# Kernel tuning notes

Measured on AMD Instinct MI355X. Metric: run time of the kernel, lower is better.

Reference implementation:

```python
import jax, jax.numpy as jnp
import numpy as np

# --- static mask-construction config (mirrors FlexAttnFunc.init_mask args) ---
B = 1
L_F, L_H, L_W = 8, 20, 36      # latent_shape[2:]
A_F, A_H, A_W = 8, 1, 1        # action_shape[2:]
PATCH = (1, 2, 2)
CHUNK = 1
PAD = 176
WINDOW = 6
DIM, HEADS, DHEAD = 1536, 12, 128
EPS = 1e-5


def _make_ids():
    lf, lh, lw = L_F // PATCH[0], L_H // PATCH[1], L_W // PATCH[2]
    lat_seq = np.repeat(np.arange(B), lf * lh * lw)
    act_seq = np.repeat(np.arange(B), A_F * A_H * A_W)
    seq = np.concatenate([lat_seq, lat_seq, act_seq, act_seq])
    lat_fr = np.broadcast_to(np.arange(L_F)[None, :, None, None], (B, L_F, lh, lw)).reshape(-1)
    act_fr = np.broadcast_to(np.arange(A_F)[None, :, None, None], (B, A_F, A_H, A_W)).reshape(-1)
    fr = np.concatenate([lat_fr // CHUNK * 2] * 2 + [act_fr // CHUNK * 2 + 1] * 2)
    nz = np.concatenate([np.zeros_like(lat_fr), np.ones_like(lat_fr),
                         np.zeros_like(act_fr), np.ones_like(act_fr)])
    pad = np.full(PAD, -1, dtype=np.int64)
    return (np.concatenate([seq, pad]).astype(np.int32),
            np.concatenate([fr, pad]).astype(np.int32),
            np.concatenate([nz, pad]).astype(np.int32))


def setup_inputs() -> dict:
    key = jax.random.key(0)
    ks = jax.random.split(key, 8)
    seq, fr, nz = _make_ids()
    S = seq.shape[0]  # 3072
    sd = 0.02
    return {
        'x': jax.random.normal(ks[0], (1, S, DIM), jnp.float32),
        'Wq': jax.random.normal(ks[1], (DIM, DIM), jnp.float32) * sd,
        'bq': jnp.zeros((DIM,), jnp.float32),
        'Wk': jax.random.normal(ks[2], (DIM, DIM), jnp.float32) * sd,
        'bk': jnp.zeros((DIM,), jnp.float32),
        'Wv': jax.random.normal(ks[3], (DIM, DIM), jnp.float32) * sd,
        'bv': jnp.zeros((DIM,), jnp.float32),
        'gq': 1.0 + jax.random.normal(ks[4], (DIM,), jnp.float32) * sd,
        'gk': 1.0 + jax.random.normal(ks[5], (DIM,), jnp.float32) * sd,
        'Wo': jax.random.normal(ks[6], (DIM, DIM), jnp.float32) * sd,
        'bo': jnp.zeros((DIM,), jnp.float32),
        'seq_ids': jnp.asarray(seq),
        'frame_ids': jnp.asarray(fr),
        'noise_ids': jnp.asarray(nz),
        'window_size': WINDOW,
    }


def _rms(u, g):
    # torch.nn.RMSNorm over last dim (size heads*dim_head), elementwise affine
    return u * jax.lax.rsqrt(jnp.mean(u * u, axis=-1, keepdims=True) + EPS) * g


def _mask(seq_ids, frame_ids, noise_ids, window_size):
    sq, sk = seq_ids[:, None], seq_ids[None, :]
    fq, fk = frame_ids[:, None], frame_ids[None, :]
    nq, nk = noise_ids[:, None], noise_ids[None, :]
    seq_ok = (sq == sk) & (sq >= 0) & (sk >= 0)
    c2c = (nq == 1) & (nk == 1) & (fk <= fq)      # clean->clean, block causal incl self
    n2c = (nq == 0) & (nk == 1) & (fk < fq)       # noise->clean, causal excl self
    n2n = (nq == 0) & (nk == 0) & (fk == fq)      # noise->noise, same frame only
    win = jnp.abs(fq - fk) <= window_size
    return (c2c | n2c | n2n) & seq_ok & win


def reference(x, Wq, bq, Wk, bk, Wv, bv, gq, gk, Wo, bo,
              seq_ids, frame_ids, noise_ids, window_size):
    S = x.shape[1]
    q = _rms(x @ Wq + bq, gq)[0].reshape(S, HEADS, DHEAD)
    k = _rms(x @ Wk + bk, gk)[0].reshape(S, HEADS, DHEAD)
    v = (x @ Wv + bv)[0].reshape(S, HEADS, DHEAD)
    mask = _mask(seq_ids, frame_ids, noise_ids, window_size)  # [S,S] bool
    scores = jnp.einsum('qhd,khd->hqk', q, k) * (DHEAD ** -0.5)
    scores = jnp.where(mask[None], scores, jnp.float32(-1e9))
    attn = jax.nn.softmax(scores, axis=-1)
    o = jnp.einsum('hqk,khd->qhd', attn, v)
    # zero out padded (fully-masked) query rows
    o = o * (seq_ids >= 0).astype(o.dtype)[:, None, None]
    y = o.reshape(1, S, HEADS * DHEAD) @ Wo + bo
    return y
```

## Files before the change

kernel.cpp:

```cpp
#include <hip/hip_runtime.h>
#include <hip/hip_bf16.h>
#include <stdint.h>

typedef __bf16 bf16x8 __attribute__((ext_vector_type(8)));
typedef float f32x4 __attribute__((ext_vector_type(4)));

__device__ __forceinline__ unsigned short f2bf(float f) {
  union { float f; unsigned int u; } v; v.f = f;
  unsigned int u = v.u;
  unsigned int r = (u + 0x7fffu + ((u >> 16) & 1u)) >> 16;
  return (unsigned short)r;
}
__device__ __forceinline__ float bf2f(unsigned short s) {
  union { unsigned int u; float f; } v; v.u = ((unsigned int)s) << 16; return v.f;
}

__global__ __launch_bounds__(256) void setup(
    const float* __restrict__ x,
    const float* __restrict__ Wq, const float* __restrict__ Wk,
    const float* __restrict__ Wv, const float* __restrict__ Wo,
    const int* __restrict__ seq, const int* __restrict__ fr,
    const int* __restrict__ nz, const int* __restrict__ wsz,
    unsigned short* __restrict__ x_bf, unsigned short* __restrict__ wt,
    unsigned long long* __restrict__ tbm, unsigned char* __restrict__ mb,
    float* __restrict__ ssq, int* __restrict__ sched, int S) {
  __shared__ __align__(16) unsigned char smu[16384];
  int b = blockIdx.x, tid = threadIdx.x;
  if (b == 0) {
    int* ks_ = (int*)smu;
    unsigned int* tm_ = (unsigned int*)(smu + 12288);
    int* cnt_s = (int*)(smu + 13312);
    int W = wsz[0];
    for (int i = tid; i < S; i += 256) {
      int sq = seq[i];
      ks_[i] = (sq < 0) ? 0 : ((1 << 9) | ((nz[i] & 1) << 8) | (fr[i] & 15) | (sq << 10));
    }
    for (int i = tid; i < 6144; i += 256) ssq[i] = 0.f;
    __syncthreads();
    for (int t = tid; t < S / 32; t += 256) {
      unsigned int m = 0;
      for (int j = 0; j < 32; j++) {
        int a = ks_[t * 32 + j];
        if (a & (1 << 9)) m |= (a & (1 << 8)) ? (1u << (16 + (a & 15))) : (1u << (a & 15));
      }
      tm_[t] = m;
    }
    __syncthreads();
    for (int qg = tid; qg < S / 16; qg += 256) {
      unsigned int allowed = 0;
      for (int j = 0; j < 16; j++) {
        int a = ks_[qg * 16 + j];
        if (!(a & (1 << 9))) continue;
        int fq = a & 15, nq = (a >> 8) & 1;
        int lo = fq - W; if (lo < 0) lo = 0;
        unsigned int lom = ~((1u << lo) - 1);
        if (nq) allowed |= (((1u << (fq + 1)) - 1) & lom) << 16;
        else    allowed |= ((((1u << fq) - 1) & lom) << 16) | (1u << fq);
      }
      unsigned long long b0 = 0, b1 = 0;
      for (int t = 0; t < 96; t++)
        if (tm_[t] & allowed) { if (t < 64) b0 |= 1ull << t; else b1 |= 1ull << (t - 64); }
      tbm[qg * 2] = b0; tbm[qg * 2 + 1] = b1;
    }
    __syncthreads();
    if (tid < 48) {
      unsigned long long u0 = tbm[(tid * 4) * 2]     | tbm[(tid * 4 + 1) * 2] |
                              tbm[(tid * 4 + 2) * 2] | tbm[(tid * 4 + 3) * 2];
      unsigned long long u1 = tbm[(tid * 4) * 2 + 1]     | tbm[(tid * 4 + 1) * 2 + 1] |
                              tbm[(tid * 4 + 2) * 2 + 1] | tbm[(tid * 4 + 3) * 2 + 1];
      cnt_s[tid] = __popcll(u0) + __popcll(u1);
    }
    __syncthreads();
    if (tid < 48) {
      int c = cnt_s[tid], rank = 0;
      for (int j = 0; j < 48; j++) {
        int cj = cnt_s[j];
        if (cj > c || (cj == c && j < tid)) rank++;
      }
      sched[rank] = tid;
    }
  } else if (b < 193) {
    int qg = b - 1;
    int* ks_ = (int*)smu;
    int W = wsz[0];
    for (int i = tid; i < S; i += 256) {
      int sq = seq[i];
      ks_[i] = (sq < 0) ? 0 : ((1 << 9) | ((nz[i] & 1) << 8) | (fr[i] & 15) | (sq << 10));
    }
    __syncthreads();
    int wave = tid >> 6, lane = tid & 63, quad = lane >> 4, l16 = lane & 15;
    int aq[4];
    for (int r = 0; r < 4; r++) aq[r] = ks_[qg * 16 + quad * 4 + r];
    for (int t = wave; t < 96; t += 4) {
      int ak[2] = { ks_[t * 32 + l16], ks_[t * 32 + 16 + l16] };
      unsigned int byte = 0;
      for (int nt = 0; nt < 2; nt++) {
        int a = ak[nt];
        int kfr = a & 15, knz = (a >> 8) & 1, kvb = (a >> 9) & 1, ksq = a >> 10;
        for (int r = 0; r < 4; r++) {
          int bq_ = aq[r];
          int qfr = bq_ & 15, qnz = (bq_ >> 8) & 1, qvb = (bq_ >> 9) & 1, qsq = bq_ >> 10;
          bool ok  = qvb && kvb && (qsq == ksq);
          bool c2c = qnz && knz && (kfr <= qfr);
          bool n2c = !qnz && knz && (kfr < qfr);
          bool n2n = !qnz && !knz && (kfr == qfr);
          int df = qfr - kfr; df = df < 0 ? -df : df;
          if ((c2c || n2c || n2n) && ok && (df <= W)) byte |= 1u << (nt * 4 + r);
        }
      }
      mb[((size_t)qg * 96 + t) * 64 + lane] = (unsigned char)byte;
    }
  } else if (b < 1345) {
    int base = (b - 193) * 1024 + tid;
    for (int j = 0; j < 4; j++) {
      int i = base + j * 256;
      float4 v = ((const float4*)x)[i];
      ushort4 o;
      o.x = f2bf(v.x); o.y = f2bf(v.y); o.z = f2bf(v.z); o.w = f2bf(v.w);
      ((ushort4*)x_bf)[i] = o;
    }
  } else {
    int id = b - 1345;
    int z = id / 576, rem = id % 576;
    int kx = rem % 24, ny = rem / 24;
    const float* W = z == 0 ? Wq : (z == 1 ? Wk : (z == 2 ? Wv : Wo));
    unsigned short (*t)[65] = (unsigned short(*)[65])smu;
    int k0 = kx * 64, n0 = ny * 64;
    const int N = 1536, K = 1536;
    for (int i = 0; i < 4; i++) {
      int e = tid + i * 256;
      int r = e >> 4, c4 = (e & 15) * 4;
      float4 v = *(const float4*)&W[(size_t)(k0 + r) * N + n0 + c4];
      t[c4 + 0][r] = f2bf(v.x);
      t[c4 + 1][r] = f2bf(v.y);
      t[c4 + 2][r] = f2bf(v.z);
      t[c4 + 3][r] = f2bf(v.w);
    }
    __syncthreads();
    for (int i = 0; i < 4; i++) {
      int e = tid + i * 256;
      int c = e >> 4, r4 = (e & 15) * 4;
      ushort4 o;
      o.x = t[c][r4 + 0];
      o.y = t[c][r4 + 1];
      o.z = t[c][r4 + 2];
      o.w = t[c][r4 + 3];
      *(ushort4*)&wt[(size_t)(z * 1536 + n0 + c) * K + k0 + r4] = o;
    }
  }
}

__global__ __launch_bounds__(512) void gemm_qkv(
    const unsigned short* __restrict__ A, const unsigned short* __restrict__ Bt,
    const float* __restrict__ bq, const float* __restrict__ bk, const float* __restrict__ bv,
    const float* __restrict__ gq, const float* __restrict__ gk,
    unsigned short* __restrict__ qt, unsigned short* __restrict__ ktb,
    unsigned short* __restrict__ vtb, float* __restrict__ ssq, int S) {
  __shared__ __align__(16) unsigned short smem[65536];
  int tid = threadIdx.x, wid = tid >> 6, lane = tid & 63;
  int quad = lane >> 4, l16 = lane & 15;
  int m0 = blockIdx.x * 256, n0 = blockIdx.y * 256;
  int wm = (wid >> 2) * 128;
  int wn = (wid & 3) * 64;
  int lr = lane >> 3;
  int lsw = ((lane & 7) ^ lr) * 8;
  int sx = l16 & 7;

  f32x4 acc[8][4] = {};

#define STAGEQ(t_, q_) do { \
    if ((t_) < 24) { \
      int b_ = (t_) & 1; \
      int k0_ = (t_) * 64; \
      unsigned short* ldsb = ((q_) < 2) ? (smem + b_ * 16384) : (smem + 32768 + b_ * 16384); \
      const unsigned short* gsrc = ((q_) < 2) ? A : Bt; \
      int rbase = ((q_) < 2) ? m0 : n0; \
      int lo8_ = ((q_) & 1) * 8; \
      for (int c_ = 0; c_ < 2; c_++) { \
        int chunk = lo8_ + c_ * 16 + wid; \
        const unsigned short* src = gsrc + (size_t)(rbase + chunk * 8 + lr) * 1536 + k0_ + lsw; \
        __builtin_amdgcn_global_load_lds( \
            (const __attribute__((address_space(1))) unsigned int*)src, \
            (__attribute__((address_space(3))) unsigned int*)(ldsb + chunk * 512 + lane * 8), 16, 0, 0); \
      } \
    } } while (0)

  STAGEQ(0, 0); STAGEQ(0, 1); STAGEQ(0, 2); STAGEQ(0, 3);
  STAGEQ(1, 0);
  asm volatile("s_waitcnt vmcnt(2)" ::: "memory");
  __builtin_amdgcn_s_barrier();
  __builtin_amdgcn_sched_barrier(0);

#define PHASE(p) do { \
    constexpr int q_ = (p) & 3; \
    constexpr int tb_ = (p) >> 2; \
    constexpr int k8_ = (q_ >> 1) * 4; \
    constexpr int mi0_ = (q_ & 1) * 4; \
    unsigned short* Ab = smem + tb_ * 16384; \
    unsigned short* Bb = smem + 32768 + tb_ * 16384; \
    int so_ = ((k8_ + quad) ^ sx) << 3; \
    if constexpr ((q_ & 1) == 0) { \
      for (int nj = 0; nj < 4; nj++) \
        bfr[nj] = *(const bf16x8*)&Bb[(wn + nj * 16 + l16) * 64 + so_]; \
    } \
    bf16x8 af[4]; \
    for (int ii = 0; ii < 4; ii++) \
      af[ii] = *(const bf16x8*)&Ab[(wm + (mi0_ + ii) * 16 + l16) * 64 + so_]; \
    STAGEQ(2 * i + kStT[p], kStQ[p]); \
    __builtin_amdgcn_sched_barrier(0); \
    __builtin_amdgcn_s_barrier(); \
    asm volatile("s_waitcnt lgkmcnt(0)" ::: "memory"); \
    __builtin_amdgcn_sched_barrier(0); \
    __builtin_amdgcn_s_setprio(1); \
    for (int ii = 0; ii < 4; ii++) \
      for (int nj = 0; nj < 4; nj++) \
        acc[mi0_ + ii][nj] = __builtin_amdgcn_mfma_f32_16x16x32_bf16(af[ii], bfr[nj], acc[mi0_ + ii][nj], 0, 0, 0); \
    __builtin_amdgcn_s_setprio(0); \
    if constexpr (q_ == 3) { asm volatile("s_waitcnt vmcnt(2)" ::: "memory"); } \
    __builtin_amdgcn_s_barrier(); \
    __builtin_amdgcn_sched_barrier(0); \
  } while (0)

  constexpr int kStT[8] = {1, 1, 1, 2, 2, 2, 2, 3};
  constexpr int kStQ[8] = {1, 2, 3, 0, 1, 2, 3, 0};

  for (int i = 0; i < 12; i++) {
    bf16x8 bfr[4];
    PHASE(0); PHASE(1); PHASE(2); PHASE(3);
    PHASE(4); PHASE(5); PHASE(6); PHASE(7);
  }
#undef PHASE
#undef STAGEQ

  int region = (n0 >= 3072) ? 2 : (n0 >= 1536 ? 1 : 0);
  int cbase = n0 - region * 1536;
  int hh0 = cbase >> 7;
  unsigned short* Cs = smem;
  if (region < 2) {
    const float* bias = region == 0 ? bq : bk;
    float* ssqp = ssq + region * 3072;
    float ss[8][4] = {};
    for (int nj = 0; nj < 4; nj++) {
      int col = wn + nj * 16 + l16;
      float b = bias[cbase + col];
      float G = (region == 1) ? gq[cbase + col] * gk[cbase + col] : 1.0f;
      for (int mi = 0; mi < 8; mi++)
        for (int r = 0; r < 4; r++) {
          float v = acc[mi][nj][r] + b;
          ss[mi][r] += v * v;
          Cs[(wm + mi * 16 + quad * 4 + r) * 256 + col] = f2bf(v * G);
        }
    }
    for (int mi = 0; mi < 8; mi++)
      for (int r = 0; r < 4; r++) {
        float v = ss[mi][r];
        for (int o = 1; o < 16; o <<= 1) v += __shfl_xor(v, o);
        if (l16 == 0)
          atomicAdd(&ssqp[m0 + wm + mi * 16 + quad * 4 + r], v);
      }
    __syncthreads();
    unsigned short* outb = (region == 0 ? qt : ktb);
    for (int p = 0; p < 16; p++) {
      int o = p * 4096 + tid * 8;
      int row = o >> 8, col = o & 255;
      size_t dst = (size_t)(hh0 + (col >> 7)) * 393216 + (size_t)(m0 + row) * 128 + (col & 127);
      *(uint4*)&outb[dst] = *(const uint4*)&Cs[o];
    }
  } else {
    for (int nj = 0; nj < 4; nj++) {
      int col = wn + nj * 16 + l16;
      float b = bv[cbase + col];
      int c8 = l16 * 8;
      for (int mi = 0; mi < 8; mi++)
        for (int r = 0; r < 4; r++) {
          int sp = wm + mi * 16 + quad * 4 + r;
          Cs[col * 256 + (sp ^ c8)] = f2bf(acc[mi][nj][r] + b);
        }
    }
    __syncthreads();
    for (int hh = 0; hh < 2; hh++) {
      unsigned short* outp = vtb + ((size_t)(hh0 + hh) * 96 + (m0 >> 5)) * 4096;
      for (int p = 0; p < 8; p++) {
        int o = p * 4096 + tid * 8;
        int tile = o >> 12, rem = o & 4095;
        int dd = rem >> 5, s31 = rem & 31;
        int laddr = (hh * 128 + dd) * 256 + ((tile * 32 + s31) ^ ((dd & 15) * 8));
        *(uint4*)&outp[o] = *(const uint4*)&Cs[laddr];
      }
    }
  }
}

__global__ __launch_bounds__(256) void gemm_wo(
    const unsigned short* __restrict__ op0b, const unsigned short* __restrict__ op1b,
    const float* __restrict__ lp, const int* __restrict__ seq,
    const unsigned short* __restrict__ Bt,
    const float* __restrict__ bias, float* __restrict__ C, int M, int N, int K) {
  __shared__ __align__(16) unsigned short smem[16384];
  unsigned short* As = smem;
  unsigned short* Bs = smem + 8192;
  int tid = threadIdx.x, wave = tid >> 6, lane = tid & 63;
  int quad = lane >> 4, l16 = lane & 15;
  int m0 = blockIdx.x * 128, n0 = blockIdx.y * 128;
  int wm = (wave & 1) * 64, wn = (wave >> 1) * 64;
  int lr = lane >> 3;
  int lc = ((lane & 7) ^ lr) * 8;
  int sx = l16 & 7;
  f32x4 acc[4][4] = {};
  for (int k0 = 0; k0 < K; k0 += 64) {
    for (int c = 0; c < 4; c++) {
      int chunk = wave * 4 + c;
      int row = chunk * 8 + lr;
      int q = m0 + row;
      int col = k0 + lc;
      int h = col >> 7, dd = col & 127;
      ushort4 a0 = *(const ushort4*)&op0b[((size_t)h * 3072 + q) * 128 + dd];
      ushort4 a1 = *(const ushort4*)&op1b[((size_t)h * 3072 + q) * 128 + dd];
      float l0 = lp[h * 3072 + q], l1 = lp[(12 + h) * 3072 + q];
      float tot = l0 + l1;
      float ok = (seq[q] >= 0 && tot > 0.f) ? 1.0f / tot : 0.0f;
      float w0 = l0 * ok, w1 = l1 * ok;
      ushort4 o;
      o.x = f2bf(bf2f(a0.x) * w0 + bf2f(a1.x) * w1);
      o.y = f2bf(bf2f(a0.y) * w0 + bf2f(a1.y) * w1);
      o.z = f2bf(bf2f(a0.z) * w0 + bf2f(a1.z) * w1);
      o.w = f2bf(bf2f(a0.w) * w0 + bf2f(a1.w) * w1);
      ushort4 a0b = *(const ushort4*)&op0b[((size_t)h * 3072 + q) * 128 + dd + 4];
      ushort4 a1b = *(const ushort4*)&op1b[((size_t)h * 3072 + q) * 128 + dd + 4];
      ushort4 o2;
      o2.x = f2bf(bf2f(a0b.x) * w0 + bf2f(a1b.x) * w1);
      o2.y = f2bf(bf2f(a0b.y) * w0 + bf2f(a1b.y) * w1);
      o2.z = f2bf(bf2f(a0b.z) * w0 + bf2f(a1b.z) * w1);
      o2.w = f2bf(bf2f(a0b.w) * w0 + bf2f(a1b.w) * w1);
      *(ushort4*)&As[chunk * 512 + lane * 8] = o;
      *(ushort4*)&As[chunk * 512 + lane * 8 + 4] = o2;
    }
    for (int c = 0; c < 4; c++) {
      int chunk = wave * 4 + c;
      int row = chunk * 8 + lr;
      const unsigned short* gb = &Bt[(size_t)(n0 + row) * K + k0 + lc];
      __builtin_amdgcn_global_load_lds(
          (const __attribute__((address_space(1))) unsigned int*)gb,
          (__attribute__((address_space(3))) unsigned int*)(Bs + chunk * 512), 16, 0, 0);
    }
    __syncthreads();
    for (int kk = 0; kk < 64; kk += 32) {
      int k8 = kk >> 3;
      int sw = ((k8 + quad) ^ sx) << 3;
      bf16x8 af[4], bfr[4];
      for (int i = 0; i < 4; i++)
        af[i] = *(const bf16x8*)&As[(wm + i * 16 + l16) * 64 + sw];
      for (int j = 0; j < 4; j++)
        bfr[j] = *(const bf16x8*)&Bs[(wn + j * 16 + l16) * 64 + sw];
      for (int i = 0; i < 4; i++)
        for (int j = 0; j < 4; j++)
          acc[i][j] = __builtin_amdgcn_mfma_f32_16x16x32_bf16(af[i], bfr[j], acc[i][j], 0, 0, 0);
    }
    __syncthreads();
  }
  for (int j = 0; j < 4; j++) {
    int col = n0 + wn + j * 16 + l16;
    float b = bias[col];
    for (int i = 0; i < 4; i++)
      for (int r = 0; r < 4; r++)
        C[(size_t)(m0 + wm + i * 16 + quad * 4 + r) * N + col] = acc[i][j][r] + b;
  }
}

__global__ __launch_bounds__(256) void attn(
    const unsigned short* __restrict__ qt,
    const unsigned short* __restrict__ kt,
    const unsigned short* __restrict__ vt,
    const unsigned char* __restrict__ mb,
    const unsigned long long* __restrict__ tbm,
    const float* __restrict__ ssq,
    const int* __restrict__ sched,
    unsigned short* __restrict__ op0b, unsigned short* __restrict__ op1b,
    float* __restrict__ lp, int S) {
  const int h = blockIdx.x;
  const int qb64 = sched[blockIdx.y];
  const int split = blockIdx.z;
  int tid = threadIdx.x, wave = tid >> 6, lane = tid & 63;
  int quad = lane >> 4, l16 = lane & 15;
  const float scale = 0.088388347648318447f;

  __shared__ __align__(16) unsigned short KsF[3 * 4096];
  __shared__ __align__(16) unsigned short VsF[3 * 4096];
  __shared__ __align__(16) unsigned short pshare[4][16][40];

  int qg = qb64 * 4 + wave;
  unsigned long long bm0 = tbm[(qb64 * 4) * 2]     | tbm[(qb64 * 4 + 1) * 2] |
                           tbm[(qb64 * 4 + 2) * 2] | tbm[(qb64 * 4 + 3) * 2];
  unsigned long long bm1 = tbm[(qb64 * 4) * 2 + 1]     | tbm[(qb64 * 4 + 1) * 2 + 1] |
                           tbm[(qb64 * 4 + 2) * 2 + 1] | tbm[(qb64 * 4 + 3) * 2 + 1];
  unsigned long long wb0 = tbm[qg * 2], wb1 = tbm[qg * 2 + 1];

  const unsigned short* kth = kt + (size_t)h * 96 * 4096;
  const unsigned short* vth = vt + (size_t)h * 96 * 4096;
  const unsigned char* mbq = mb + (size_t)qg * 96 * 64;

  bf16x8 qf[4];
  {
    const unsigned short* qp = qt + ((size_t)(h * 192 + qg) * 16 + l16) * 128 + quad * 8;
    for (int ks = 0; ks < 4; ks++) qf[ks] = *(const bf16x8*)&qp[ks * 32];
  }
  float qs[4];
  for (int r = 0; r < 4; r++) {
    int row = qb64 * 64 + wave * 16 + quad * 4 + r;
    qs[r] = rsqrtf(ssq[row] * (1.0f / 1536.0f) + 1e-5f) * scale;
  }
  const float* ssk = ssq + 3072;

  f32x4 oacc[8] = {};
  f32x4 lacc = {};
  const __bf16 onebf = (__bf16)1.0f;
  const bf16x8 ones = {onebf, onebf, onebf, onebf, onebf, onebf, onebf, onebf};

#define POP(dst) do { \
    if (bm0) { dst = __builtin_ctzll(bm0); bm0 &= bm0 - 1; } \
    else if (bm1) { dst = 64 + __builtin_ctzll(bm1); bm1 &= bm1 - 1; } \
    else dst = -1; } while (0)

#define STAGE(t_, b_) do { \
    for (int j = 0; j < 2; j++) { \
      int slot = j * 256 + tid; \
      int key = slot >> 4, cc = slot & 15; \
      const unsigned short* src = kth + (size_t)(t_) * 4096 + key * 128 + (cc ^ (key & 15)) * 8; \
      __builtin_amdgcn_global_load_lds( \
          (const __attribute__((address_space(1))) unsigned int*)src, \
          (__attribute__((address_space(3))) unsigned int*)(&KsF[(b_) * 4096] + j * 2048 + wave * 512), \
          16, 0, 0); \
    } \
    for (int j = 0; j < 2; j++) { \
      int slot = j * 256 + tid; \
      int row = slot >> 2, cc = slot & 3; \
      const unsigned short* src = vth + (size_t)(t_) * 4096 + row * 32 + (cc ^ ((row >> 1) & 3)) * 8; \
      __builtin_amdgcn_global_load_lds( \
          (const __attribute__((address_space(1))) unsigned int*)src, \
          (__attribute__((address_space(3))) unsigned int*)(&VsF[(b_) * 4096] + j * 2048 + wave * 512), \
          16, 0, 0); \
    } } while (0)

  int tA, tB, dsc;
  if (split) POP(dsc);
  POP(tA);
  unsigned int mbA = 0, mbB = 0;
  float aS0 = 0.f, aS1 = 0.f, bS0 = 0.f, bS1 = 0.f;
  if (tA >= 0) {
    STAGE(tA, 0);
    mbA = mbq[tA * 64 + lane];
    aS0 = ssk[tA * 32 + l16]; aS1 = ssk[tA * 32 + 16 + l16];
  }
  POP(dsc); POP(tB);
  if (tB >= 0) {
    STAGE(tB, 1);
    mbB = mbq[tB * 64 + lane];
    bS0 = ssk[tB * 32 + l16]; bS1 = ssk[tB * 32 + 16 + l16];
  }
  int bufA = 0, bufB = 1, bufC = 2;

  while (tA >= 0) {
    if (tB >= 0) { asm volatile("s_waitcnt vmcnt(7)" ::: "memory"); }
    else         { asm volatile("s_waitcnt vmcnt(0)" ::: "memory"); }
    __builtin_amdgcn_s_barrier();
    __builtin_amdgcn_sched_barrier(0);

    int tC; POP(dsc); POP(tC);
    unsigned int mbC = 0; float cS0 = 0.f, cS1 = 0.f;
    if (tC >= 0) {
      STAGE(tC, bufC);
      mbC = mbq[tC * 64 + lane];
      cS0 = ssk[tC * 32 + l16]; cS1 = ssk[tC * 32 + 16 + l16];
    }
    __builtin_amdgcn_sched_barrier(0);

    bool live = (tA < 64) ? ((wb0 >> tA) & 1) : ((wb1 >> (tA - 64)) & 1);
    if (live) {
      const unsigned short* Kb = &KsF[bufA * 4096];
      const unsigned short* Vb = &VsF[bufA * 4096];
      f32x4 sacc[2] = {};
      __builtin_amdgcn_s_setprio(1);
      for (int nt = 0; nt < 2; nt++) {
        int key = nt * 16 + l16;
        for (int ks = 0; ks < 4; ks++) {
          int cc = (ks * 4 + quad) ^ l16;
          bf16x8 kf = *(const bf16x8*)&Kb[(key * 16 + cc) * 8];
          sacc[nt] = __builtin_amdgcn_mfma_f32_16x16x32_bf16(qf[ks], kf, sacc[nt], 0, 0, 0);
        }
      }
      __builtin_amdgcn_s_setprio(0);
      float ksc[2];
      ksc[0] = rsqrtf(aS0 * (1.0f / 1536.0f) + 1e-5f);
      ksc[1] = rsqrtf(aS1 * (1.0f / 1536.0f) + 1e-5f);
      for (int nt = 0; nt < 2; nt++)
        for (int r = 0; r < 4; r++) {
          float e = __expf(sacc[nt][r] * (qs[r] * ksc[nt]) - 16.0f);
          float p = ((mbA >> (nt * 4 + r)) & 1) ? e : 0.0f;
          pshare[wave][quad * 4 + r][nt * 16 + l16] = f2bf(p);
        }
      __asm__ __volatile__("s_waitcnt lgkmcnt(0)" ::: "memory");
      bf16x8 pf = *(const bf16x8*)&pshare[wave][l16][quad * 8];
      __builtin_amdgcn_s_setprio(1);
      for (int d = 0; d < 8; d++) {
        int row = d * 16 + l16;
        int cc = quad ^ ((l16 >> 1) & 3);
        bf16x8 vf = *(const bf16x8*)&Vb[(row * 4 + cc) * 8];
        oacc[d] = __builtin_amdgcn_mfma_f32_16x16x32_bf16(pf, vf, oacc[d], 0, 0, 0);
      }
      lacc = __builtin_amdgcn_mfma_f32_16x16x32_bf16(pf, ones, lacc, 0, 0, 0);
      __builtin_amdgcn_s_setprio(0);
    }
    tA = tB; tB = tC;
    mbA = mbB; mbB = mbC;
    aS0 = bS0; aS1 = bS1; bS0 = cS0; bS1 = cS1;
    int tmpb = bufA; bufA = bufB; bufB = bufC; bufC = tmpb;
  }
#undef POP
#undef STAGE

  unsigned short* po = split ? op1b : op0b;
  for (int r = 0; r < 4; r++) {
    int q = qb64 * 64 + wave * 16 + quad * 4 + r;
    float inv = (lacc[r] > 0.f) ? 1.0f / lacc[r] : 0.0f;
    for (int d = 0; d < 8; d++)
      po[((size_t)h * S + q) * 128 + d * 16 + l16] = f2bf(oacc[d][r] * inv);
    if (l16 == 0)
      lp[((size_t)split * 12 + h) * S + q] = lacc[r];
  }
}

extern "C" void kernel_launch(void* const* d_in, const int* in_sizes, int n_in,
                              void* d_out, int out_size, void* d_ws, size_t ws_size,
                              hipStream_t stream) {
  const float* x  = (const float*)d_in[0];
  const float* Wq = (const float*)d_in[1];
  const float* bq = (const float*)d_in[2];
  const float* Wk = (const float*)d_in[3];
  const float* bk = (const float*)d_in[4];
  const float* Wv = (const float*)d_in[5];
  const float* bv = (const float*)d_in[6];
  const float* gq = (const float*)d_in[7];
  const float* gk = (const float*)d_in[8];
  const float* Wo = (const float*)d_in[9];
  const float* bo = (const float*)d_in[10];
  const int* seq  = (const int*)d_in[11];
  const int* fr   = (const int*)d_in[12];
  const int* nz   = (const int*)d_in[13];
  const int* wsz  = (const int*)d_in[14];
  float* out = (float*)d_out;
  const int S = in_sizes[11];
  const int D = 1536;

  char* ws = (char*)d_ws;
  size_t off = 0;
  unsigned short* x_bf = (unsigned short*)(ws + off); off += (size_t)S * D * 2;
  unsigned short* wt   = (unsigned short*)(ws + off); off += (size_t)4 * D * D * 2;
  unsigned short* qt   = (unsigned short*)(ws + off); off += (size_t)S * D * 2;
  unsigned short* ktb  = (unsigned short*)(ws + off); off += (size_t)S * D * 2;
  unsigned short* vtb  = (unsigned short*)(ws + off); off += (size_t)S * D * 2;
  unsigned short* op0b = (unsigned short*)(ws + off); off += (size_t)S * D * 2;
  unsigned short* op1b = (unsigned short*)(ws + off); off += (size_t)S * D * 2;
  unsigned long long* tbm = (unsigned long long*)(ws + off); off += (size_t)(S / 16) * 16;
  unsigned char*  mbuf = (unsigned char*)(ws + off);  off += (size_t)(S / 16) * 96 * 64;
  float*          lp   = (float*)(ws + off);          off += (size_t)2 * 12 * S * 4;
  float*          ssq  = (float*)(ws + off);          off += (size_t)2 * 3072 * 4;
  int*            schd = (int*)(ws + off);            off += 64 * 4;

  dim3 blk(256);
  setup<<<dim3(3649), blk, 0, stream>>>(x, Wq, Wk, Wv, Wo, seq, fr, nz, wsz,
                                        x_bf, wt, tbm, mbuf, ssq, schd, S);
  gemm_qkv<<<dim3(S / 256, 3 * D / 256), dim3(512), 0, stream>>>(x_bf, wt, bq, bk, bv, gq, gk,
                                                                 qt, ktb, vtb, ssq, S);
  attn<<<dim3(D / 128, S / 64, 2), blk, 0, stream>>>(qt, ktb, vtb, mbuf, tbm, ssq, schd,
                                                     op0b, op1b, lp, S);
  gemm_wo<<<dim3(S / 128, D / 128), blk, 0, stream>>>(op0b, op1b, lp, seq,
                                                      wt + (size_t)3 * D * D,
                                                      bo, out, S, D, D);
}
```

Measured before the change: 282.9 us.

## Software-pipeline split-merge operand loads in Wo GEMM and transpose lse layout

The Wo GEMM now prefetches the next K-slice's two attention partial outputs and their row sums into registers while the current slice is merged and multiplied. It issues wider 16-byte loads, waits with explicit vmcnt counts and raw barriers, and raises wave priority around the MFMA block. The attention kernel now writes the per-row sums in a row-major [q][24] layout so each GEMM row reads its values from nearby addresses. The aim is to hide global-load latency for the A operand behind compute, at the cost of more registers and hand-tuned waitcnt values that could be wrong.

```diff
diff --git a/kernel.cpp b/kernel.cpp
--- a/kernel.cpp
+++ b/kernel.cpp
@@ -293,7 +293,7 @@
 
 __global__ __launch_bounds__(256) void gemm_wo(
     const unsigned short* __restrict__ op0b, const unsigned short* __restrict__ op1b,
-    const float* __restrict__ lp, const int* __restrict__ seq,
+    const float* __restrict__ lpT, const int* __restrict__ seq,
     const unsigned short* __restrict__ Bt,
     const float* __restrict__ bias, float* __restrict__ C, int M, int N, int K) {
   __shared__ __align__(16) unsigned short smem[16384];
@@ -306,35 +306,32 @@
   int lr = lane >> 3;
   int lc = ((lane & 7) ^ lr) * 8;
   int sx = l16 & 7;
+
+  int qrow[4];
+  float gate[4];
+  for (int c = 0; c < 4; c++) {
+    qrow[c] = m0 + (wave * 4 + c) * 8 + lr;
+    gate[c] = (seq[qrow[c]] >= 0) ? 1.0f : 0.0f;
+  }
+
   f32x4 acc[4][4] = {};
+  uint4 p0[4], p1[4];
+  float pl0[4], pl1[4];
+
+#define PREF(k0_) do { \
+    int h_ = (k0_) >> 7; \
+    int dd_ = ((k0_) & 64) + lc; \
+    for (int c = 0; c < 4; c++) { \
+      size_t base_ = ((size_t)h_ * 3072 + qrow[c]) * 128 + dd_; \
+      p0[c] = *(const uint4*)&op0b[base_]; \
+      p1[c] = *(const uint4*)&op1b[base_]; \
+      pl0[c] = lpT[qrow[c] * 24 + h_]; \
+      pl1[c] = lpT[qrow[c] * 24 + 12 + h_]; \
+    } } while (0)
+
+  PREF(0);
+  __builtin_amdgcn_sched_barrier(0);
   for (int k0 = 0; k0 < K; k0 += 64) {
-    for (int c = 0; c < 4; c++) {
-      int chunk = wave * 4 + c;
-      int row = chunk * 8 + lr;
-      int q = m0 + row;
-      int col = k0 + lc;
-      int h = col >> 7, dd = col & 127;
-      ushort4 a0 = *(const ushort4*)&op0b[((size_t)h * 3072 + q) * 128 + dd];
-      ushort4 a1 = *(const ushort4*)&op1b[((size_t)h * 3072 + q) * 128 + dd];
-      float l0 = lp[h * 3072 + q], l1 = lp[(12 + h) * 3072 + q];
-      float tot = l0 + l1;
-      float ok = (seq[q] >= 0 && tot > 0.f) ? 1.0f / tot : 0.0f;
-      float w0 = l0 * ok, w1 = l1 * ok;
-      ushort4 o;
-      o.x = f2bf(bf2f(a0.x) * w0 + bf2f(a1.x) * w1);
-      o.y = f2bf(bf2f(a0.y) * w0 + bf2f(a1.y) * w1);
-      o.z = f2bf(bf2f(a0.z) * w0 + bf2f(a1.z) * w1);
-      o.w = f2bf(bf2f(a0.w) * w0 + bf2f(a1.w) * w1);
-      ushort4 a0b = *(const ushort4*)&op0b[((size_t)h * 3072 + q) * 128 + dd + 4];
-      ushort4 a1b = *(const ushort4*)&op1b[((size_t)h * 3072 + q) * 128 + dd + 4];
-      ushort4 o2;
-      o2.x = f2bf(bf2f(a0b.x) * w0 + bf2f(a1b.x) * w1);
-      o2.y = f2bf(bf2f(a0b.y) * w0 + bf2f(a1b.y) * w1);
-      o2.z = f2bf(bf2f(a0b.z) * w0 + bf2f(a1b.z) * w1);
-      o2.w = f2bf(bf2f(a0b.w) * w0 + bf2f(a1b.w) * w1);
-      *(ushort4*)&As[chunk * 512 + lane * 8] = o;
-      *(ushort4*)&As[chunk * 512 + lane * 8 + 4] = o2;
-    }
     for (int c = 0; c < 4; c++) {
       int chunk = wave * 4 + c;
       int row = chunk * 8 + lr;
@@ -343,7 +340,37 @@
           (const __attribute__((address_space(1))) unsigned int*)gb,
           (__attribute__((address_space(3))) unsigned int*)(Bs + chunk * 512), 16, 0, 0);
     }
-    __syncthreads();
+    __builtin_amdgcn_sched_barrier(0);
+    for (int c = 0; c < 4; c++) {
+      int chunk = wave * 4 + c;
+      float tot = pl0[c] + pl1[c];
+      float ok = (gate[c] != 0.0f && tot > 0.f) ? 1.0f / tot : 0.0f;
+      float w0 = pl0[c] * ok, w1 = pl1[c] * ok;
+      unsigned int u0[4], u1[4], ro[4];
+      u0[0] = p0[c].x; u0[1] = p0[c].y; u0[2] = p0[c].z; u0[3] = p0[c].w;
+      u1[0] = p1[c].x; u1[1] = p1[c].y; u1[2] = p1[c].z; u1[3] = p1[c].w;
+      for (int j = 0; j < 4; j++) {
+        float lo = bf2f((unsigned short)(u0[j] & 0xffffu)) * w0 +
+                   bf2f((unsigned short)(u1[j] & 0xffffu)) * w1;
+        float hi = bf2f((unsigned short)(u0[j] >> 16)) * w0 +
+                   bf2f((unsigned short)(u1[j] >> 16)) * w1;
+        ro[j] = (unsigned int)f2bf(lo) | ((unsigned int)f2bf(hi) << 16);
+      }
+      uint4 w;
+      w.x = ro[0]; w.y = ro[1]; w.z = ro[2]; w.w = ro[3];
+      *(uint4*)&As[chunk * 512 + lane * 8] = w;
+    }
+    __builtin_amdgcn_sched_barrier(0);
+    if (k0 + 64 < K) {
+      PREF(k0 + 64);
+      __builtin_amdgcn_sched_barrier(0);
+      asm volatile("s_waitcnt vmcnt(12)" ::: "memory");
+    } else {
+      asm volatile("s_waitcnt vmcnt(0)" ::: "memory");
+    }
+    asm volatile("s_waitcnt lgkmcnt(0)" ::: "memory");
+    __builtin_amdgcn_s_barrier();
+    __builtin_amdgcn_sched_barrier(0);
     for (int kk = 0; kk < 64; kk += 32) {
       int k8 = kk >> 3;
       int sw = ((k8 + quad) ^ sx) << 3;
@@ -352,12 +379,16 @@
         af[i] = *(const bf16x8*)&As[(wm + i * 16 + l16) * 64 + sw];
       for (int j = 0; j < 4; j++)
         bfr[j] = *(const bf16x8*)&Bs[(wn + j * 16 + l16) * 64 + sw];
+      __builtin_amdgcn_s_setprio(1);
       for (int i = 0; i < 4; i++)
         for (int j = 0; j < 4; j++)
           acc[i][j] = __builtin_amdgcn_mfma_f32_16x16x32_bf16(af[i], bfr[j], acc[i][j], 0, 0, 0);
-    }
-    __syncthreads();
-  }
+      __builtin_amdgcn_s_setprio(0);
+    }
+    __builtin_amdgcn_s_barrier();
+    __builtin_amdgcn_sched_barrier(0);
+  }
+#undef PREF
   for (int j = 0; j < 4; j++) {
     int col = n0 + wn + j * 16 + l16;
     float b = bias[col];
@@ -525,7 +556,7 @@
     for (int d = 0; d < 8; d++)
       po[((size_t)h * S + q) * 128 + d * 16 + l16] = f2bf(oacc[d][r] * inv);
     if (l16 == 0)
-      lp[((size_t)split * 12 + h) * S + q] = lacc[r];
+      lp[(size_t)q * 24 + split * 12 + h] = lacc[r];
   }
 }
 
```

Measured after the change: 284.1 us. No clear change (+0.4%).
